# Optimization experiments

Hardware: AMD Instinct MI355X
Metric: run time of the kernel (lower is better)

The kernel has to match this reference:

```python
import jax, jax.numpy as jnp
import numpy as np

B, PD, CD = 8192, 1024, 1024


def setup_inputs() -> dict:
    key = jax.random.key(0)
    ks = jax.random.split(key, 10)
    u = lambda k, shape: jax.random.uniform(k, shape, dtype=jnp.float32, minval=-0.05, maxval=0.05)
    return {
        "P": jax.random.normal(ks[0], (B, PD), dtype=jnp.float32),
        "C1": jax.random.normal(ks[1], (B, CD), dtype=jnp.float32),
        "C2": jax.random.normal(ks[2], (B, CD), dtype=jnp.float32),
        "C3": jax.random.normal(ks[3], (B, CD), dtype=jnp.float32),
        "C4": jax.random.normal(ks[4], (B, CD), dtype=jnp.float32),
        "GateWeight_P": u(ks[5], (PD, CD)),
        "GateWeight_C": u(ks[6], (CD, CD)),
        "GateBias": u(ks[7], (CD,)),
        "OutWeight": u(ks[8], (PD, CD)),
        "OutBias": u(ks[9], (CD, 1)),
    }


def reference(P, C1, C2, C3, C4, GateWeight_P, GateWeight_C, GateBias, OutWeight, OutBias):
    # Stack the 4 choice branches: [4, B, C]
    Cs = jnp.stack([C1, C2, C3, C4], axis=0)
    WP = P @ GateWeight_P                                  # [B, C]
    WC = jnp.einsum("kbc,cd->kbd", Cs, GateWeight_C)       # [4, B, C]
    g = jax.nn.sigmoid(WP[None] + WC + GateBias)           # [4, B, C]
    C_dash = Cs * g                                        # [4, B, C]
    WP_out = P @ OutWeight                                 # [B, C]
    scores = jnp.einsum("kbc,bc->kb", C_dash, WP_out)      # batch_dot axes=[1,1]
    bias = jnp.einsum("kbc,c->kb", C_dash, OutBias[:, 0])  # K.dot(C_dash, OutBias)
    return (scores + bias).T                               # [B, 4]
```

## Files before the change

### kernel.cpp

```cpp
#include <hip/hip_runtime.h>
#include <hip/hip_bf16.h>


#define B_  8192
#define PD_ 1024
#define CD_ 1024

typedef unsigned short ushort_t;
typedef unsigned int   uint_t;
typedef __attribute__((ext_vector_type(8))) short    short8;
typedef __attribute__((ext_vector_type(4))) float    floatx4;

__device__ __forceinline__ float bf2f(unsigned short u) {
    return __uint_as_float(((unsigned)u) << 16);
}
__device__ __forceinline__ unsigned short f2bf(float f) {
    unsigned u = __float_as_uint(f);
    unsigned r = u + 0x7FFFu + ((u >> 16) & 1u);
    return (unsigned short)(r >> 16);
}

__global__ __launch_bounds__(256) void prep_kernel(const float* __restrict__ P,
                                                   const float* __restrict__ C1,
                                                   const float* __restrict__ C2,
                                                   const float* __restrict__ C3,
                                                   const float* __restrict__ C4,
                                                   const float* __restrict__ GWP,
                                                   const float* __restrict__ OW,
                                                   const float* __restrict__ GWC,
                                                   ushort_t* __restrict__ Pb,
                                                   ushort_t* __restrict__ Call,
                                                   ushort_t* __restrict__ Wcat,
                                                   ushort_t* __restrict__ GWCt,
                                                   float* __restrict__ out) {
    const int bid = blockIdx.x;
    const int tid = threadIdx.x;
    if (bid < 40960) {
        const int seg = bid >> 13;
        const int i   = (bid & 8191) * 256 + tid;
        const float* src;
        ushort_t* dst;
        switch (seg) {
            case 0: src = P;  dst = Pb; break;
            case 1: src = C1; dst = Call; break;
            case 2: src = C2; dst = Call + (size_t)1 * B_ * CD_; break;
            case 3: src = C3; dst = Call + (size_t)2 * B_ * CD_; break;
            default: src = C4; dst = Call + (size_t)3 * B_ * CD_; break;
        }
        float4 v = ((const float4*)src)[i];
        ushort4 o;
        o.x = f2bf(v.x); o.y = f2bf(v.y); o.z = f2bf(v.z); o.w = f2bf(v.w);
        ((ushort4*)dst)[i] = o;
    } else if (bid < 44032) {
        __shared__ float tile[32][33];
        const int tb  = bid - 40960;
        const int seg = tb >> 10;
        const int t32 = tb & 1023;
        const float* src;
        ushort_t* dst;
        switch (seg) {
            case 0: src = GWP; dst = Wcat; break;
            case 1: src = OW;  dst = Wcat + 1024 * 1024; break;
            default: src = GWC; dst = GWCt; break;
        }
        const int c0 = (t32 & 31) * 32, r0 = (t32 >> 5) * 32;
        const int x = tid & 31, y = tid >> 5;
        for (int i = y; i < 32; i += 8)
            tile[i][x] = src[(size_t)(r0 + i) * 1024 + c0 + x];
        __syncthreads();
        for (int i = y; i < 32; i += 8)
            dst[(size_t)(c0 + i) * 1024 + r0 + x] = f2bf(tile[x][i]);
    } else {
        const int i = (bid - 44032) * 256 + tid;
        ((float4*)out)[i] = float4{0.f, 0.f, 0.f, 0.f};
    }
}

__device__ __forceinline__ void gl_lds16(const void* g, void* l) {
    __builtin_amdgcn_global_load_lds((const __attribute__((address_space(1))) void*)g,
                                     (__attribute__((address_space(3))) void*)l, 16, 0, 0);
}

__global__ __launch_bounds__(256, 4) void gemmA(const ushort_t* __restrict__ A,
                                                const ushort_t* __restrict__ Bt,
                                                ushort_t* __restrict__ C) {
    __shared__ ushort_t smem[8192];
    ushort_t* lA = smem;
    ushort_t* lB = smem + 4096;
    const int K = 1024;
    const int xcd = blockIdx.x & 7, q = blockIdx.x >> 3;
    const int tileM = ((q >> 4) * 8 + xcd) * 128;
    const int tileN = (q & 15) * 128;

    const int t = threadIdx.x;
    const int wave = t >> 6, lane = t & 63;
    const int quad = lane >> 4, l16 = lane & 15;
    const int wm = wave >> 1, wn = wave & 1;

    const int srow = t >> 2;
    const int sc   = ((t & 3) ^ ((t >> 3) & 3)) * 8;
    const ushort_t* Ag = A  + (size_t)(tileM + srow) * K + sc;
    const ushort_t* Bg = Bt + (size_t)(tileN + srow) * K + sc;
    const int lo = t * 8;
    const int fro = (l16 * 4 + (quad ^ ((l16 >> 1) & 3))) * 8;

    floatx4 acc[4][4];
#pragma unroll
    for (int i = 0; i < 4; i++)
#pragma unroll
        for (int j = 0; j < 4; j++) acc[i][j] = (floatx4)0.f;

    for (int k0 = 0; k0 < K; k0 += 32) {
        gl_lds16(Ag + k0,                   &lA[lo]);
        gl_lds16(Ag + (size_t)64 * K + k0,  &lA[lo + 2048]);
        gl_lds16(Bg + k0,                   &lB[lo]);
        gl_lds16(Bg + (size_t)64 * K + k0,  &lB[lo + 2048]);
        __syncthreads();
        short8 af[4], bfr[4];
#pragma unroll
        for (int mi = 0; mi < 4; mi++)
            af[mi] = *(const short8*)&lA[(wm * 4 + mi) * 512 + fro];
#pragma unroll
        for (int ni = 0; ni < 4; ni++)
            bfr[ni] = *(const short8*)&lB[(wn * 4 + ni) * 512 + fro];
#pragma unroll
        for (int mi = 0; mi < 4; mi++)
#pragma unroll
            for (int ni = 0; ni < 4; ni++)
                acc[mi][ni] = __builtin_amdgcn_mfma_f32_16x16x32_bf16(
                    af[mi], bfr[ni], acc[mi][ni], 0, 0, 0);
        __syncthreads();
    }
#pragma unroll
    for (int mi = 0; mi < 4; mi++)
#pragma unroll
        for (int ni = 0; ni < 4; ni++) {
            const int col = tileN + wn * 64 + ni * 16 + l16;
            const int ci = col & 1023, hi = col >> 10;
#pragma unroll
            for (int r = 0; r < 4; r++) {
                const int row = tileM + wm * 64 + mi * 16 + quad * 4 + r;
                C[(size_t)(row * 1024 + ci) * 2 + hi] = f2bf(acc[mi][ni][r]);
            }
        }
}

__global__ __launch_bounds__(256, 4) void gemmB_fused(const ushort_t* __restrict__ Call,
                                                      const ushort_t* __restrict__ GWCt,
                                                      const uint_t* __restrict__ WPcat,
                                                      const float* __restrict__ Gb,
                                                      const float* __restrict__ Ob,
                                                      float* __restrict__ out) {
    __shared__ ushort_t smem[8192];
    ushort_t* lA = smem;
    ushort_t* lB = smem + 4096;
    const int K = 1024;
    const int xcd = blockIdx.x & 7, q = blockIdx.x >> 3;
    const int tileM = ((q >> 3) * 8 + xcd) * 128;
    const int tileN = (q & 7) * 128;

    const int t = threadIdx.x;
    const int wave = t >> 6, lane = t & 63;
    const int quad = lane >> 4, l16 = lane & 15;
    const int wm = wave >> 1, wn = wave & 1;

    const int srow = t >> 2;
    const int sc   = ((t & 3) ^ ((t >> 3) & 3)) * 8;
    const ushort_t* Ag = Call + (size_t)(tileM + srow) * K + sc;
    const ushort_t* Bg = GWCt + (size_t)(tileN + srow) * K + sc;
    const int lo = t * 8;
    const int fro = (l16 * 4 + (quad ^ ((l16 >> 1) & 3))) * 8;

    floatx4 acc[4][4];
#pragma unroll
    for (int i = 0; i < 4; i++)
#pragma unroll
        for (int j = 0; j < 4; j++) acc[i][j] = (floatx4)0.f;

    for (int k0 = 0; k0 < K; k0 += 32) {
        gl_lds16(Ag + k0,                   &lA[lo]);
        gl_lds16(Ag + (size_t)64 * K + k0,  &lA[lo + 2048]);
        gl_lds16(Bg + k0,                   &lB[lo]);
        gl_lds16(Bg + (size_t)64 * K + k0,  &lB[lo + 2048]);
        __syncthreads();
        short8 af[4], bfr[4];
#pragma unroll
        for (int mi = 0; mi < 4; mi++)
            af[mi] = *(const short8*)&lA[(wm * 4 + mi) * 512 + fro];
#pragma unroll
        for (int ni = 0; ni < 4; ni++)
            bfr[ni] = *(const short8*)&lB[(wn * 4 + ni) * 512 + fro];
#pragma unroll
        for (int mi = 0; mi < 4; mi++)
#pragma unroll
            for (int ni = 0; ni < 4; ni++)
                acc[mi][ni] = __builtin_amdgcn_mfma_f32_16x16x32_bf16(
                    af[mi], bfr[ni], acc[mi][ni], 0, 0, 0);
        __syncthreads();
    }

    const int kk   = tileM >> 13;
    const int b0   = (tileM & 8191) + wm * 64 + quad * 4;
    const int rowg = tileM + wm * 64 + quad * 4;

    float gbv[4], obv[4];
    int   gcol[4];
#pragma unroll
    for (int ni = 0; ni < 4; ni++) {
        gcol[ni] = tileN + wn * 64 + ni * 16 + l16;
        gbv[ni]  = Gb[gcol[ni]];
        obv[ni]  = Ob[gcol[ni]];
    }

#pragma unroll
    for (int mi = 0; mi < 4; mi++) {
        float part[4] = {0.f, 0.f, 0.f, 0.f};
#pragma unroll
        for (int ni = 0; ni < 4; ni++) {
            const uint_t*   wpp = WPcat + (size_t)(b0 + mi * 16) * 1024 + gcol[ni];
            const ushort_t* ckp = Call  + (size_t)(rowg + mi * 16) * 1024 + gcol[ni];
#pragma unroll
            for (int r = 0; r < 4; r++) {
                const uint_t wpair = wpp[(size_t)r * 1024];
                const float wp  = bf2f((unsigned short)(wpair & 0xffffu));
                const float wpo = bf2f((unsigned short)(wpair >> 16));
                const float ck  = bf2f(ckp[(size_t)r * 1024]);
                const float x = wp + acc[mi][ni][r] + gbv[ni];
                const float g = 1.f / (1.f + __expf(-x));
                part[r] += ck * g * (wpo + obv[ni]);
            }
        }
#pragma unroll
        for (int r = 0; r < 4; r++) {
            part[r] += __shfl_xor(part[r], 1);
            part[r] += __shfl_xor(part[r], 2);
            part[r] += __shfl_xor(part[r], 4);
            part[r] += __shfl_xor(part[r], 8);
        }
        if (l16 == 0) {
#pragma unroll
            for (int r = 0; r < 4; r++)
                atomicAdd(&out[(size_t)(b0 + mi * 16 + r) * 4 + kk], part[r]);
        }
    }
}

extern "C" void kernel_launch(void* const* d_in, const int* in_sizes, int n_in,
                              void* d_out, int out_size, void* d_ws, size_t ws_size,
                              hipStream_t stream) {
    (void)in_sizes; (void)n_in; (void)out_size; (void)ws_size;
    const float* P   = (const float*)d_in[0];
    const float* C1  = (const float*)d_in[1];
    const float* C2  = (const float*)d_in[2];
    const float* C3  = (const float*)d_in[3];
    const float* C4  = (const float*)d_in[4];
    const float* GWP = (const float*)d_in[5];
    const float* GWC = (const float*)d_in[6];
    const float* Gb  = (const float*)d_in[7];
    const float* OW  = (const float*)d_in[8];
    const float* Ob  = (const float*)d_in[9];
    float* out = (float*)d_out;

    char* ws = (char*)d_ws;
    ushort_t* Pb    = (ushort_t*)(ws);
    ushort_t* Call  = (ushort_t*)(ws + (16u << 20));
    ushort_t* Wcat  = (ushort_t*)(ws + (80u << 20));
    ushort_t* GWCt  = (ushort_t*)(ws + (84u << 20));
    ushort_t* WPcat = (ushort_t*)(ws + (86u << 20));

    prep_kernel<<<44064, 256, 0, stream>>>(P, C1, C2, C3, C4, GWP, OW, GWC,
                                           Pb, Call, Wcat, GWCt, out);
    gemmA<<<1024, 256, 0, stream>>>(Pb, Wcat, WPcat);
    gemmB_fused<<<2048, 256, 0, stream>>>(Call, GWCt, (const uint_t*)WPcat, Gb, Ob, out);
}
```

Measured before the change: 347.2 us.

## Stash C tiles in LDS during K-loop and split WP outputs into planar arrays

```diff
diff --git a/kernel.cpp b/kernel.cpp
--- a/kernel.cpp
+++ b/kernel.cpp
@@ -7,7 +7,6 @@
 #define CD_ 1024
 
 typedef unsigned short ushort_t;
-typedef unsigned int   uint_t;
 typedef __attribute__((ext_vector_type(8))) short    short8;
 typedef __attribute__((ext_vector_type(4))) float    floatx4;
 
@@ -83,7 +82,8 @@
 
 __global__ __launch_bounds__(256, 4) void gemmA(const ushort_t* __restrict__ A,
                                                 const ushort_t* __restrict__ Bt,
-                                                ushort_t* __restrict__ C) {
+                                                ushort_t* __restrict__ Wp,
+                                                ushort_t* __restrict__ Wpo) {
     __shared__ ushort_t smem[8192];
     ushort_t* lA = smem;
     ushort_t* lB = smem + 4096;
@@ -131,27 +131,30 @@
                     af[mi], bfr[ni], acc[mi][ni], 0, 0, 0);
         __syncthreads();
     }
+
+    ushort_t* Cw = (tileN < 1024) ? Wp : Wpo;
+    const int cb = tileN & 1023;
 #pragma unroll
     for (int mi = 0; mi < 4; mi++)
 #pragma unroll
         for (int ni = 0; ni < 4; ni++) {
-            const int col = tileN + wn * 64 + ni * 16 + l16;
-            const int ci = col & 1023, hi = col >> 10;
+            const int col = cb + wn * 64 + ni * 16 + l16;
 #pragma unroll
             for (int r = 0; r < 4; r++) {
                 const int row = tileM + wm * 64 + mi * 16 + quad * 4 + r;
-                C[(size_t)(row * 1024 + ci) * 2 + hi] = f2bf(acc[mi][ni][r]);
+                Cw[(size_t)row * 1024 + col] = f2bf(acc[mi][ni][r]);
             }
         }
 }
 
-__global__ __launch_bounds__(256, 4) void gemmB_fused(const ushort_t* __restrict__ Call,
+__global__ __launch_bounds__(256, 3) void gemmB_fused(const ushort_t* __restrict__ Call,
                                                       const ushort_t* __restrict__ GWCt,
-                                                      const uint_t* __restrict__ WPcat,
+                                                      const ushort_t* __restrict__ Wp,
+                                                      const ushort_t* __restrict__ Wpo,
                                                       const float* __restrict__ Gb,
                                                       const float* __restrict__ Ob,
                                                       float* __restrict__ out) {
-    __shared__ ushort_t smem[8192];
+    __shared__ ushort_t smem[24576];
     ushort_t* lA = smem;
     ushort_t* lB = smem + 4096;
     const int K = 1024;
@@ -170,6 +173,7 @@
     const ushort_t* Bg = GWCt + (size_t)(tileN + srow) * K + sc;
     const int lo = t * 8;
     const int fro = (l16 * 4 + (quad ^ ((l16 >> 1) & 3))) * 8;
+    const int kt0s = tileN >> 5;
 
     floatx4 acc[4][4];
 #pragma unroll
@@ -182,6 +186,11 @@
         gl_lds16(Ag + (size_t)64 * K + k0,  &lA[lo + 2048]);
         gl_lds16(Bg + k0,                   &lB[lo]);
         gl_lds16(Bg + (size_t)64 * K + k0,  &lB[lo + 2048]);
+        const unsigned dw = (unsigned)((k0 >> 5) - kt0s);
+        if (dw < 4u) {
+            gl_lds16(Ag + k0,                  &smem[8192 + dw * 4096 + lo]);
+            gl_lds16(Ag + (size_t)64 * K + k0, &smem[8192 + dw * 4096 + lo + 2048]);
+        }
         __syncthreads();
         short8 af[4], bfr[4];
 #pragma unroll
@@ -201,7 +210,6 @@
 
     const int kk   = tileM >> 13;
     const int b0   = (tileM & 8191) + wm * 64 + quad * 4;
-    const int rowg = tileM + wm * 64 + quad * 4;
 
     float gbv[4], obv[4];
     int   gcol[4];
@@ -217,14 +225,17 @@
         float part[4] = {0.f, 0.f, 0.f, 0.f};
 #pragma unroll
         for (int ni = 0; ni < 4; ni++) {
-            const uint_t*   wpp = WPcat + (size_t)(b0 + mi * 16) * 1024 + gcol[ni];
-            const ushort_t* ckp = Call  + (size_t)(rowg + mi * 16) * 1024 + gcol[ni];
+            const int k_local = ((ni & 1) << 4) + l16;
+            const int widx    = wn * 2 + (ni >> 1);
+            const ushort_t* wpp  = Wp  + (size_t)(b0 + mi * 16) * 1024 + gcol[ni];
+            const ushort_t* wpop = Wpo + (size_t)(b0 + mi * 16) * 1024 + gcol[ni];
 #pragma unroll
             for (int r = 0; r < 4; r++) {
-                const uint_t wpair = wpp[(size_t)r * 1024];
-                const float wp  = bf2f((unsigned short)(wpair & 0xffffu));
-                const float wpo = bf2f((unsigned short)(wpair >> 16));
-                const float ck  = bf2f(ckp[(size_t)r * 1024]);
+                const int rowp = wm * 64 + mi * 16 + quad * 4 + r;
+                const int slot = (k_local >> 3) ^ ((rowp >> 1) & 3);
+                const float ck = bf2f(smem[8192 + widx * 4096 + rowp * 32 + slot * 8 + (k_local & 7)]);
+                const float wp  = bf2f(wpp[(size_t)r * 1024]);
+                const float wpo = bf2f(wpop[(size_t)r * 1024]);
                 const float x = wp + acc[mi][ni][r] + gbv[ni];
                 const float g = 1.f / (1.f + __expf(-x));
                 part[r] += ck * g * (wpo + obv[ni]);
@@ -266,10 +277,11 @@
     ushort_t* Call  = (ushort_t*)(ws + (16u << 20));
     ushort_t* Wcat  = (ushort_t*)(ws + (80u << 20));
     ushort_t* GWCt  = (ushort_t*)(ws + (84u << 20));
-    ushort_t* WPcat = (ushort_t*)(ws + (86u << 20));
+    ushort_t* Wp    = (ushort_t*)(ws + (86u << 20));
+    ushort_t* Wpo   = (ushort_t*)(ws + (102u << 20));
 
     prep_kernel<<<44064, 256, 0, stream>>>(P, C1, C2, C3, C4, GWP, OW, GWC,
                                            Pb, Call, Wcat, GWCt, out);
-    gemmA<<<1024, 256, 0, stream>>>(Pb, Wcat, WPcat);
-    gemmB_fused<<<2048, 256, 0, stream>>>(Call, GWCt, (const uint_t*)WPcat, Gb, Ob, out);
-}
+    gemmA<<<1024, 256, 0, stream>>>(Pb, Wcat, Wp, Wpo);
+    gemmB_fused<<<2048, 256, 0, stream>>>(Call, GWCt, Wp, Wpo, Gb, Ob, out);
+}
```

Result: no change. 350.4 us (+0.9%).
